# Performance work log

Hardware: AMD Instinct MI355X
Metric: run time of the kernel (lower is better)

## Reference

```python
import jax, jax.numpy as jnp
import numpy as np

B, N, D, H = 2, 512, 256, 256  # batch, seq_len, input_dim, hidden_dim
H2 = H // 2


def setup_inputs() -> dict:
    key = jax.random.key(0)
    ks = jax.random.split(key, 12)
    def lin(kw, kb, fan_in, fan_out):
        bound = 1.0 / np.sqrt(fan_in)
        W = jax.random.uniform(kw, (fan_in, fan_out), jnp.float32, -bound, bound)
        b = jax.random.uniform(kb, (fan_out,), jnp.float32, -bound, bound)
        return W, b
    W1, b1 = lin(ks[0], ks[1], 2 * D, H)
    W2, b2 = lin(ks[2], ks[3], H, H2)
    W3, b3 = lin(ks[4], ks[5], H2, 1)
    Wg, bg = lin(ks[6], ks[7], D, H)
    x = jax.random.normal(ks[8], (B, N, D), jnp.float32)
    base_adj = jax.random.uniform(ks[9], (B, N, N), jnp.float32)
    return {"x": x, "base_adj": base_adj, "W1": W1, "b1": b1,
            "W2": W2, "b2": b2, "W3": W3, "b3": b3, "Wg": Wg, "bg": bg}


def reference(x, base_adj, W1, b1, W2, b2, W3, b3, Wg, bg):
    # x: [B,N,D], base_adj: [B,N,N]
    Din = x.shape[-1]
    n = x.shape[1]
    # Linear on concat([x_i, x_j]) == x_i @ W1[:D] + x_j @ W1[D:]  (same math,
    # avoids materializing the [B,N,N,2D] pair tensor)
    left = jnp.einsum('bid,dh->bih', x, W1[:Din])    # [B,N,H]
    right = jnp.einsum('bjd,dh->bjh', x, W1[Din:])   # [B,N,H]
    h = jax.nn.relu(left[:, :, None, :] + right[:, None, :, :] + b1)  # [B,N,N,H]
    h = jax.nn.relu(jnp.einsum('bijh,hk->bijk', h, W2) + b2)          # [B,N,N,H/2]
    edge_weights = jax.nn.sigmoid(jnp.einsum('bijk,k->bij', h, W3[:, 0]) + b3[0])
    dynamic_adj = base_adj * edge_weights + jnp.eye(n, dtype=x.dtype)[None]
    dynamic_adj = jax.nn.softmax(dynamic_adj, axis=-1)
    agg = jnp.matmul(dynamic_adj, x)                 # [B,N,D]
    return jnp.einsum('bnd,dh->bnh', agg, Wg) + bg   # [B,N,H]
```

## Files before the change

kernel.cpp:

```cpp
#include <hip/hip_runtime.h>
#include <hip/hip_bf16.h>

#define NB 2
#define NN 512
#define ND 256
#define NH 256
#define NH2 128
#define JT 32

typedef __bf16 bf16x8 __attribute__((ext_vector_type(8)));
typedef __bf16 bf16x4 __attribute__((ext_vector_type(4)));
typedef float f32x4 __attribute__((ext_vector_type(4)));

__device__ __forceinline__ float bflo(unsigned d) { return __uint_as_float(d << 16); }
__device__ __forceinline__ float bfhi(unsigned d) { return __uint_as_float(d & 0xffff0000u); }

__device__ __forceinline__ void buildHs(char* dst, const uint4* rg4, const float* l8,
                                        unsigned hsOff) {
  #pragma unroll
  for (int it = 0; it < 4; ++it) {
    const uint4 rv = rg4[it];
    bf16x8 hb;
    #pragma unroll
    for (int e = 0; e < 4; ++e) {
      const unsigned d = ((const unsigned*)&rv)[e];
      float t0 = bflo(d) + l8[2 * e];
      float t1 = bfhi(d) + l8[2 * e + 1];
      t0 = t0 > 0.f ? t0 : 0.f;
      t1 = t1 > 0.f ? t1 : 0.f;
      hb[2 * e] = (__bf16)t0;
      hb[2 * e + 1] = (__bf16)t1;
    }
    *(bf16x8*)(dst + hsOff + it * 4096) = hb;
  }
}

__global__ __launch_bounds__(256) void prep_kernel(
    const float* __restrict__ x, const float* __restrict__ W1,
    const float* __restrict__ b1, const float* __restrict__ Wg,
    const float* __restrict__ bg, const float* __restrict__ W2,
    float* __restrict__ Lb, __bf16* __restrict__ Rb16,
    __bf16* __restrict__ XWt, __bf16* __restrict__ W2b) {
  const int blk = blockIdx.x;
  const int tid = threadIdx.x;
  __shared__ float xs[2][ND];
  __shared__ __align__(16) f32x4 part[4 * 384];
  const int r0 = blk * 2;
  xs[0][tid] = x[r0 * ND + tid];
  xs[1][tid] = x[(r0 + 1) * ND + tid];
  if (tid < 64) {
    const int idx = blk * 64 + tid;
    const int hh = idx >> 7, kk = idx & 127;
    W2b[kk * NH + hh] = (__bf16)W2[idx];
  }
  __syncthreads();

  const int dg = tid >> 6;
  const int hq = tid & 63;
  f32x4 acc[2][3];
  #pragma unroll
  for (int r = 0; r < 2; ++r)
    #pragma unroll
    for (int m = 0; m < 3; ++m) acc[r][m] = (f32x4){0.f, 0.f, 0.f, 0.f};

  const int d0 = dg * 64;
  #pragma unroll 4
  for (int it = 0; it < 64; ++it) {
    const int d = d0 + it;
    const f32x4 wl = *(const f32x4*)(W1 + d * NH + hq * 4);
    const f32x4 wr = *(const f32x4*)(W1 + (ND + d) * NH + hq * 4);
    const f32x4 wg = *(const f32x4*)(Wg + d * NH + hq * 4);
    const float x0 = xs[0][d], x1 = xs[1][d];
    acc[0][0] += x0 * wl;  acc[0][1] += x0 * wr;  acc[0][2] += x0 * wg;
    acc[1][0] += x1 * wl;  acc[1][1] += x1 * wr;  acc[1][2] += x1 * wg;
  }
  #pragma unroll
  for (int r = 0; r < 2; ++r)
    #pragma unroll
    for (int m = 0; m < 3; ++m)
      part[dg * 384 + (r * 3 + m) * 64 + hq] = acc[r][m];
  __syncthreads();

  for (int s = tid; s < 384; s += 256) {
    f32x4 sum = part[s] + part[384 + s] + part[768 + s] + part[1152 + s];
    const int r = s / 192;
    const int rem = s - r * 192;
    const int m = rem >> 6;
    const int h = (rem & 63) * 4;
    const int row = r0 + r;
    if (m == 0) {
      const f32x4 bv = *(const f32x4*)(b1 + h);
      *(f32x4*)(Lb + row * NH + h) = sum + bv;
    } else if (m == 1) {
      bf16x4 o;
      #pragma unroll
      for (int e = 0; e < 4; ++e) o[e] = (__bf16)sum[e];
      *(bf16x4*)(Rb16 + row * NH + h) = o;
    } else {
      const f32x4 v = sum + *(const f32x4*)(bg + h);
      const int bb = row >> 9, jj = row & (NN - 1);
      #pragma unroll
      for (int e = 0; e < 4; ++e)
        XWt[bb * (NH * NN) + (h + e) * NN + jj] = (__bf16)v[e];
    }
  }
}

__global__ __launch_bounds__(256, 4) void edge_kernel(
    const float* __restrict__ base_adj,
    const float* __restrict__ b2, const float* __restrict__ W3,
    const float* __restrict__ b3, const float* __restrict__ Lb,
    const __bf16* __restrict__ Rb16, const __bf16* __restrict__ XWt,
    const __bf16* __restrict__ W2b, float* __restrict__ out) {
  __shared__ __align__(16) char HsB[32768];
  __shared__ __align__(16) float adjs[NN];
  __shared__ __align__(16) float ew[NN];
  __shared__ float red[2][4][JT];
  __shared__ float b2s[NH2], W3s[NH2];
  __shared__ float sred[8];

  const int blk = blockIdx.x;
  const int tid = threadIdx.x;
  const int lane = tid & 63;
  const int w = tid >> 6;
  const int lr = lane & 15;
  const int lg = lane >> 4;
  const int b = blk >> 9;
  const int i = blk & (NN - 1);

  adjs[tid] = base_adj[(b * NN + i) * NN + tid];
  adjs[tid + 256] = base_adj[(b * NN + i) * NN + tid + 256];
  if (tid < NH2) { b2s[tid] = b2[tid]; W3s[tid] = W3[tid]; }
  const float b3v = b3[0];

  const __bf16* Rbb = Rb16 + b * NN * NH;
  const __bf16* XWtb = XWt + b * NH * NN;

  const int cth = tid & 31;
  const int rowth = tid >> 5;
  const unsigned hsOff = rowth * 512 + ((cth ^ (rowth & 7)) << 4);

  float l8[8];
  {
    const f32x4 la = *(const f32x4*)(Lb + blk * NH + cth * 8);
    const f32x4 lc = *(const f32x4*)(Lb + blk * NH + cth * 8 + 4);
    #pragma unroll
    for (int e = 0; e < 4; ++e) { l8[e] = la[e]; l8[4 + e] = lc[e]; }
  }

  bf16x8 bfr[8][2];
  #pragma unroll
  for (int ks8 = 0; ks8 < 8; ++ks8)
    #pragma unroll
    for (int kb = 0; kb < 2; ++kb)
      bfr[ks8][kb] = *(const bf16x8*)(W2b + (w * 32 + kb * 16 + lr) * NH + ks8 * 32 + lg * 8);

  uint4 rg4[4];
  #pragma unroll
  for (int it = 0; it < 4; ++it)
    rg4[it] = *(const uint4*)(Rbb + (it * 8 + rowth) * NH + cth * 8);
  buildHs(HsB, rg4, l8, hsOff);
  #pragma unroll
  for (int it = 0; it < 4; ++it)
    rg4[it] = *(const uint4*)(Rbb + (JT + it * 8 + rowth) * NH + cth * 8);
  __syncthreads();

  for (int jt = 0; jt < 16; ++jt) {
    const int buf = jt & 1;
    const char* Hp = HsB + buf * 16384;
    f32x4 acc[2][2];
    #pragma unroll
    for (int ja = 0; ja < 2; ++ja)
      #pragma unroll
      for (int kb = 0; kb < 2; ++kb) acc[ja][kb] = (f32x4){0.f, 0.f, 0.f, 0.f};
    #pragma unroll
    for (int ks8 = 0; ks8 < 8; ++ks8) {
      bf16x8 af[2];
      #pragma unroll
      for (int ja = 0; ja < 2; ++ja)
        af[ja] = *(const bf16x8*)(Hp + (ja * 16 + lr) * 512 + (((ks8 * 4 + lg) ^ (lr & 7)) << 4));
      #pragma unroll
      for (int ja = 0; ja < 2; ++ja)
        #pragma unroll
        for (int kb = 0; kb < 2; ++kb)
          acc[ja][kb] = __builtin_amdgcn_mfma_f32_16x16x32_bf16(af[ja], bfr[ks8][kb], acc[ja][kb], 0, 0, 0);
    }
    #pragma unroll
    for (int ja = 0; ja < 2; ++ja) {
      #pragma unroll
      for (int r = 0; r < 4; ++r) {
        const int k0 = w * 32 + lr;
        float t0 = acc[ja][0][r] + b2s[k0];
        float t1 = acc[ja][1][r] + b2s[k0 + 16];
        t0 = t0 > 0.f ? t0 : 0.f;
        t1 = t1 > 0.f ? t1 : 0.f;
        float s = fmaf(t0, W3s[k0], t1 * W3s[k0 + 16]);
        s += __shfl_xor(s, 1, 16);
        s += __shfl_xor(s, 2, 16);
        s += __shfl_xor(s, 4, 16);
        s += __shfl_xor(s, 8, 16);
        if (lr == 0) red[buf][w][ja * 16 + lg * 4 + r] = s;
      }
    }
    if (jt < 15) buildHs(HsB + (buf ^ 1) * 16384, rg4, l8, hsOff);
    if (jt < 14) {
      #pragma unroll
      for (int it = 0; it < 4; ++it)
        rg4[it] = *(const uint4*)(Rbb + ((jt + 2) * JT + it * 8 + rowth) * NH + cth * 8);
    }
    __syncthreads();
    if (tid < JT) {
      const float v = red[buf][0][tid] + red[buf][1][tid] + red[buf][2][tid] +
                      red[buf][3][tid] + b3v;
      const float sg = 1.f / (1.f + __expf(-v));
      const int j = jt * JT + tid;
      ew[j] = adjs[j] * sg + ((j == i) ? 1.f : 0.f);
    }
  }
  __syncthreads();

  float v0 = ew[tid], v1 = ew[tid + 256];
  float m = fmaxf(v0, v1);
  #pragma unroll
  for (int off = 1; off < 64; off <<= 1) m = fmaxf(m, __shfl_xor(m, off, 64));
  if (lane == 0) sred[w] = m;
  __syncthreads();
  m = fmaxf(fmaxf(sred[0], sred[1]), fmaxf(sred[2], sred[3]));
  const float e0 = __expf(v0 - m), e1 = __expf(v1 - m);
  float ssum = e0 + e1;
  #pragma unroll
  for (int off = 1; off < 64; off <<= 1) ssum += __shfl_xor(ssum, off, 64);
  if (lane == 0) sred[4 + w] = ssum;
  __syncthreads();
  const float inv = 1.f / (sred[4] + sred[5] + sred[6] + sred[7]);
  const float p0 = e0 * inv, p1 = e1 * inv;

  __bf16* ewh = (__bf16*)ew;
  __bf16* ewl = ewh + NN;
  {
    const __bf16 h0 = (__bf16)p0;
    const __bf16 h1 = (__bf16)p1;
    ewh[tid] = h0;        ewl[tid] = (__bf16)(p0 - (float)h0);
    ewh[tid + 256] = h1;  ewl[tid + 256] = (__bf16)(p1 - (float)h1);
  }
  __syncthreads();

  const char* ewb = (const char*)ew;
  const unsigned aoff = (lr == 1 ? 1024u : 0u) + lg * 16;
  const bool azero = (lr >= 2);
  f32x4 pacc[4];
  #pragma unroll
  for (int q = 0; q < 4; ++q) pacc[q] = (f32x4){0.f, 0.f, 0.f, 0.f};
  #pragma unroll
  for (int ks = 0; ks < 16; ++ks) {
    uint4 pa = *(const uint4*)(ewb + aoff + ks * 64);
    if (azero) { pa.x = 0; pa.y = 0; pa.z = 0; pa.w = 0; }
    const bf16x8 paf = __builtin_bit_cast(bf16x8, pa);
    #pragma unroll
    for (int q = 0; q < 4; ++q) {
      const int h = w * 64 + q * 16 + lr;
      const bf16x8 bv = *(const bf16x8*)(XWtb + h * NN + ks * 32 + lg * 8);
      pacc[q] = __builtin_amdgcn_mfma_f32_16x16x32_bf16(paf, bv, pacc[q], 0, 0, 0);
    }
  }
  if (lg == 0) {
    #pragma unroll
    for (int q = 0; q < 4; ++q)
      out[blk * NH + w * 64 + q * 16 + lr] = pacc[q][0] + pacc[q][1];
  }
}

extern "C" void kernel_launch(void* const* d_in, const int* in_sizes, int n_in,
                              void* d_out, int out_size, void* d_ws, size_t ws_size,
                              hipStream_t stream) {
  const float* x        = (const float*)d_in[0];
  const float* base_adj = (const float*)d_in[1];
  const float* W1       = (const float*)d_in[2];
  const float* b1       = (const float*)d_in[3];
  const float* W2       = (const float*)d_in[4];
  const float* b2       = (const float*)d_in[5];
  const float* W3       = (const float*)d_in[6];
  const float* b3       = (const float*)d_in[7];
  const float* Wg       = (const float*)d_in[8];
  const float* bg       = (const float*)d_in[9];

  float*  Lb    = (float*)d_ws;
  __bf16* Rb16  = (__bf16*)(Lb + NB * NN * NH);
  __bf16* XWt   = Rb16 + NB * NN * NH;
  __bf16* W2b   = XWt + NB * NH * NN;
  float* outp = (float*)d_out;

  prep_kernel<<<512, 256, 0, stream>>>(x, W1, b1, Wg, bg, W2, Lb, Rb16, XWt, W2b);
  edge_kernel<<<NB * NN, 256, 0, stream>>>(base_adj, b2, W3, b3, Lb, Rb16, XWt, W2b, outp);
}
```

Baseline: 184.6 us.

## Stream R tiles via direct global-to-LDS loads with single-buffered H tile

Replaces register-staged prefetch of the R tile with async global_load_lds copies into an LDS staging buffer, then builds the ReLU'd H tile from LDS each iteration. This frees the rg4 registers and drops the double-buffered H tile, which may allow higher occupancy. It also stages Lb through LDS and raises wave priority around the MFMA loop. The cost is an extra barrier per tile, and H construction is no longer overlapped with the previous tile's compute.

```diff
diff --git a/kernel.cpp b/kernel.cpp
--- a/kernel.cpp
+++ b/kernel.cpp
@@ -12,28 +12,12 @@
 typedef __bf16 bf16x4 __attribute__((ext_vector_type(4)));
 typedef float f32x4 __attribute__((ext_vector_type(4)));
 
+__device__ __forceinline__ void gload_lds16(const void* g, void* l) {
+  __builtin_amdgcn_global_load_lds((const __attribute__((address_space(1))) unsigned int*)g,
+                                   (__attribute__((address_space(3))) unsigned int*)l, 16, 0, 0);
+}
 __device__ __forceinline__ float bflo(unsigned d) { return __uint_as_float(d << 16); }
 __device__ __forceinline__ float bfhi(unsigned d) { return __uint_as_float(d & 0xffff0000u); }
-
-__device__ __forceinline__ void buildHs(char* dst, const uint4* rg4, const float* l8,
-                                        unsigned hsOff) {
-  #pragma unroll
-  for (int it = 0; it < 4; ++it) {
-    const uint4 rv = rg4[it];
-    bf16x8 hb;
-    #pragma unroll
-    for (int e = 0; e < 4; ++e) {
-      const unsigned d = ((const unsigned*)&rv)[e];
-      float t0 = bflo(d) + l8[2 * e];
-      float t1 = bfhi(d) + l8[2 * e + 1];
-      t0 = t0 > 0.f ? t0 : 0.f;
-      t1 = t1 > 0.f ? t1 : 0.f;
-      hb[2 * e] = (__bf16)t0;
-      hb[2 * e + 1] = (__bf16)t1;
-    }
-    *(bf16x8*)(dst + hsOff + it * 4096) = hb;
-  }
-}
 
 __global__ __launch_bounds__(256) void prep_kernel(
     const float* __restrict__ x, const float* __restrict__ W1,
@@ -112,10 +96,12 @@
     const float* __restrict__ b3, const float* __restrict__ Lb,
     const __bf16* __restrict__ Rb16, const __bf16* __restrict__ XWt,
     const __bf16* __restrict__ W2b, float* __restrict__ out) {
-  __shared__ __align__(16) char HsB[32768];
+  __shared__ __align__(16) __bf16 Rs[JT * NH];
+  __shared__ __align__(16) __bf16 Hs[JT * NH];
+  __shared__ __align__(16) float Lbs[NH];
   __shared__ __align__(16) float adjs[NN];
   __shared__ __align__(16) float ew[NN];
-  __shared__ float red[2][4][JT];
+  __shared__ float red[4][JT];
   __shared__ float b2s[NH2], W3s[NH2];
   __shared__ float sred[8];
 
@@ -128,63 +114,89 @@
   const int b = blk >> 9;
   const int i = blk & (NN - 1);
 
+  const __bf16* Rbb = Rb16 + b * NN * NH;
+  const __bf16* XWtb = XWt + b * NH * NN;
+
+  {
+    const int laneoff = (lane >> 5) * NH + (lane & 31) * 8;
+    #pragma unroll
+    for (int q = 0; q < 4; ++q) {
+      const __bf16* src = Rbb + (w * 4 + q) * 2 * NH + laneoff;
+      gload_lds16(src, (char*)Rs + (w * 4 + q) * 1024);
+    }
+  }
+  bf16x8 bfr[8][2];
+  #pragma unroll
+  for (int ks8 = 0; ks8 < 8; ++ks8)
+    #pragma unroll
+    for (int kb = 0; kb < 2; ++kb)
+      bfr[ks8][kb] = *(const bf16x8*)(W2b + (w * 32 + kb * 16 + lr) * NH + ks8 * 32 + lg * 8);
+
+  Lbs[tid] = Lb[blk * NH + tid];
   adjs[tid] = base_adj[(b * NN + i) * NN + tid];
   adjs[tid + 256] = base_adj[(b * NN + i) * NN + tid + 256];
   if (tid < NH2) { b2s[tid] = b2[tid]; W3s[tid] = W3[tid]; }
   const float b3v = b3[0];
-
-  const __bf16* Rbb = Rb16 + b * NN * NH;
-  const __bf16* XWtb = XWt + b * NH * NN;
+  asm volatile("s_waitcnt vmcnt(0)" ::: "memory");
+  __syncthreads();
 
   const int cth = tid & 31;
   const int rowth = tid >> 5;
-  const unsigned hsOff = rowth * 512 + ((cth ^ (rowth & 7)) << 4);
-
   float l8[8];
-  {
-    const f32x4 la = *(const f32x4*)(Lb + blk * NH + cth * 8);
-    const f32x4 lc = *(const f32x4*)(Lb + blk * NH + cth * 8 + 4);
-    #pragma unroll
-    for (int e = 0; e < 4; ++e) { l8[e] = la[e]; l8[4 + e] = lc[e]; }
-  }
-
-  bf16x8 bfr[8][2];
-  #pragma unroll
-  for (int ks8 = 0; ks8 < 8; ++ks8)
-    #pragma unroll
-    for (int kb = 0; kb < 2; ++kb)
-      bfr[ks8][kb] = *(const bf16x8*)(W2b + (w * 32 + kb * 16 + lr) * NH + ks8 * 32 + lg * 8);
-
-  uint4 rg4[4];
-  #pragma unroll
-  for (int it = 0; it < 4; ++it)
-    rg4[it] = *(const uint4*)(Rbb + (it * 8 + rowth) * NH + cth * 8);
-  buildHs(HsB, rg4, l8, hsOff);
-  #pragma unroll
-  for (int it = 0; it < 4; ++it)
-    rg4[it] = *(const uint4*)(Rbb + (JT + it * 8 + rowth) * NH + cth * 8);
-  __syncthreads();
+  #pragma unroll
+  for (int e = 0; e < 8; ++e) l8[e] = Lbs[cth * 8 + e];
+  const unsigned rsAddr0 = tid * 16;
+  const unsigned hsAddr0 = rowth * 512 + ((cth ^ (rowth & 7)) << 4);
 
   for (int jt = 0; jt < 16; ++jt) {
-    const int buf = jt & 1;
-    const char* Hp = HsB + buf * 16384;
+    #pragma unroll
+    for (int it = 0; it < 4; ++it) {
+      const uint4 rv = *(const uint4*)((const char*)Rs + rsAddr0 + it * 4096);
+      bf16x8 hb;
+      #pragma unroll
+      for (int e = 0; e < 4; ++e) {
+        const unsigned d = ((const unsigned*)&rv)[e];
+        float t0 = bflo(d) + l8[2 * e];
+        float t1 = bfhi(d) + l8[2 * e + 1];
+        t0 = t0 > 0.f ? t0 : 0.f;
+        t1 = t1 > 0.f ? t1 : 0.f;
+        hb[2 * e] = (__bf16)t0;
+        hb[2 * e + 1] = (__bf16)t1;
+      }
+      *(bf16x8*)((char*)Hs + hsAddr0 + it * 4096) = hb;
+    }
+    __syncthreads();
+
+    if (jt < 15) {
+      const int laneoff = (lane >> 5) * NH + (lane & 31) * 8;
+      const __bf16* base = Rbb + (jt + 1) * (JT * NH);
+      #pragma unroll
+      for (int q = 0; q < 4; ++q) {
+        const __bf16* src = base + (w * 4 + q) * 2 * NH + laneoff;
+        gload_lds16(src, (char*)Rs + (w * 4 + q) * 1024);
+      }
+    }
+
     f32x4 acc[2][2];
     #pragma unroll
     for (int ja = 0; ja < 2; ++ja)
       #pragma unroll
       for (int kb = 0; kb < 2; ++kb) acc[ja][kb] = (f32x4){0.f, 0.f, 0.f, 0.f};
+    __builtin_amdgcn_s_setprio(1);
     #pragma unroll
     for (int ks8 = 0; ks8 < 8; ++ks8) {
       bf16x8 af[2];
       #pragma unroll
       for (int ja = 0; ja < 2; ++ja)
-        af[ja] = *(const bf16x8*)(Hp + (ja * 16 + lr) * 512 + (((ks8 * 4 + lg) ^ (lr & 7)) << 4));
+        af[ja] = *(const bf16x8*)((const char*)Hs + (ja * 16 + lr) * 512 + (((ks8 * 4 + lg) ^ (lr & 7)) << 4));
       #pragma unroll
       for (int ja = 0; ja < 2; ++ja)
         #pragma unroll
         for (int kb = 0; kb < 2; ++kb)
           acc[ja][kb] = __builtin_amdgcn_mfma_f32_16x16x32_bf16(af[ja], bfr[ks8][kb], acc[ja][kb], 0, 0, 0);
     }
+    __builtin_amdgcn_s_setprio(0);
+
     #pragma unroll
     for (int ja = 0; ja < 2; ++ja) {
       #pragma unroll
@@ -199,19 +211,14 @@
         s += __shfl_xor(s, 2, 16);
         s += __shfl_xor(s, 4, 16);
         s += __shfl_xor(s, 8, 16);
-        if (lr == 0) red[buf][w][ja * 16 + lg * 4 + r] = s;
+        if (lr == 0) red[w][ja * 16 + lg * 4 + r] = s;
       }
     }
-    if (jt < 15) buildHs(HsB + (buf ^ 1) * 16384, rg4, l8, hsOff);
-    if (jt < 14) {
-      #pragma unroll
-      for (int it = 0; it < 4; ++it)
-        rg4[it] = *(const uint4*)(Rbb + ((jt + 2) * JT + it * 8 + rowth) * NH + cth * 8);
-    }
+    asm volatile("s_waitcnt vmcnt(0)" ::: "memory");
     __syncthreads();
+
     if (tid < JT) {
-      const float v = red[buf][0][tid] + red[buf][1][tid] + red[buf][2][tid] +
-                      red[buf][3][tid] + b3v;
+      const float v = red[0][tid] + red[1][tid] + red[2][tid] + red[3][tid] + b3v;
       const float sg = 1.f / (1.f + __expf(-v));
       const int j = jt * JT + tid;
       ew[j] = adjs[j] * sg + ((j == i) ? 1.f : 0.f);
```

Measured after the change: 176.7 us. 1.04x faster.
